# Performance work log

Measured on AMD Instinct MI355X. Metric: run time of the kernel, lower is better.

## Reference

```python
import jax, jax.numpy as jnp
import numpy as np

HIDDEN = 1024
NUM_HEADS = 8
HEAD_DIM = HIDDEN // NUM_HEADS
ROPE_BASE = 10000.0
RMS_EPS = 1e-6


def _rotate_half(x):
    # interleaved rotate: (x0,x1,x2,x3,...) -> (-x1,x0,-x3,x2,...)
    x1 = x[..., ::2]
    x2 = x[..., 1::2]
    return jnp.stack([-x2, x1], axis=-1).reshape(x.shape)


def _rope_cos_sin(seq_len, rotary_dim, dtype):
    inv_freq = 1.0 / (ROPE_BASE ** (jnp.arange(0, rotary_dim, 2, dtype=jnp.float32) / rotary_dim))
    pos = jnp.arange(seq_len, dtype=jnp.float32)
    freqs = pos[:, None] * inv_freq[None, :]            # [S, rd/2]
    cos = jnp.repeat(jnp.cos(freqs), 2, axis=-1)        # [S, rd]
    sin = jnp.repeat(jnp.sin(freqs), 2, axis=-1)
    return cos.astype(dtype)[None, None], sin.astype(dtype)[None, None]


def setup_inputs() -> dict:
    key = jax.random.key(0)
    k = jax.random.split(key, 8)
    B, S, H = 2, 2048, HIDDEN
    hidden_states = jax.random.normal(k[0], (B, S, H), dtype=jnp.float32)
    attention_mask = jax.random.randint(k[1], (B, S, S), 0, 2) > 0
    rel_ts_bias = jax.random.normal(k[2], (B, S, S), dtype=jnp.float32)
    s1 = 1.0 / np.sqrt(H)
    W_qkvu = jax.random.normal(k[3], (H, H * 6), dtype=jnp.float32) * s1
    W_out = jax.random.normal(k[4], (H * 3, H), dtype=jnp.float32) * (1.0 / np.sqrt(H * 3))
    b_out = jnp.zeros((H,), dtype=jnp.float32)
    rms_weight = jnp.ones((H,), dtype=jnp.float32)
    return {"hidden_states": hidden_states, "attention_mask": attention_mask,
            "rel_ts_bias": rel_ts_bias, "W_qkvu": W_qkvu, "W_out": W_out,
            "b_out": b_out, "rms_weight": rms_weight}


def reference(hidden_states, attention_mask, rel_ts_bias, W_qkvu, W_out, b_out, rms_weight):
    B, S, H = hidden_states.shape
    nh, hd = NUM_HEADS, HEAD_DIM
    fused = jax.nn.silu(hidden_states @ W_qkvu)          # [B,S,6H]
    gated = fused[..., :3 * H]                            # [B,S,3H]
    v = fused[..., 3 * H:4 * H].reshape(B, S, nh, hd).transpose(0, 2, 1, 3)
    q = fused[..., 4 * H:5 * H].reshape(B, S, nh, hd).transpose(0, 2, 1, 3)
    kk = fused[..., 5 * H:].reshape(B, S, nh, hd).transpose(0, 2, 1, 3)

    cos, sin = _rope_cos_sin(S, hd, hidden_states.dtype)  # rotary_dim == head_dim
    q_rope = q * cos + _rotate_half(q) * sin
    k_rope = kk * cos + _rotate_half(kk) * sin

    inv_s = 1.0 / max(S, 1)
    qk = jax.nn.relu(jnp.einsum('bhnd,bhmd->bhnm', q, kk)) * inv_s
    qk_rope = jax.nn.relu(jnp.einsum('bhnd,bhmd->bhnm', q_rope, k_rope)) * inv_s

    mask = attention_mask[:, None]                        # [B,1,S,S]
    qk = jnp.where(mask, qk, 0.0)
    qk_rope = jnp.where(mask, qk_rope, 0.0)
    ts_bias = jnp.where(attention_mask, rel_ts_bias, 0.0)

    ts_out = jnp.einsum('bnm,bhmd->bnhd', ts_bias, v)
    rope_out = jnp.einsum('bhnm,bhmd->bnhd', qk_rope, v)
    plain_out = jnp.einsum('bhnm,bhmd->bnhd', qk, v)

    combined = jnp.concatenate([rope_out, ts_out, plain_out], axis=-1).reshape(B, S, 3 * H)
    out = (combined * gated) @ W_out + b_out
    y = out + hidden_states
    rms = jax.lax.rsqrt(jnp.mean(y * y, axis=-1, keepdims=True) + RMS_EPS)
    return y * rms * rms_weight
```

## Files before the change

### kernel.cpp

```cpp
#include <hip/hip_runtime.h>
#include <math.h>

static constexpr int Bz = 2;
static constexpr int Sq = 2048;
static constexpr int Hh = 1024;
static constexpr int NH = 8;
static constexpr int HD = 128;
static constexpr int H3 = 3072;
static constexpr int H6 = 6144;

typedef unsigned short ushort_t;
typedef float f32x4v __attribute__((ext_vector_type(4)));
typedef short s16x8 __attribute__((ext_vector_type(8)));

static constexpr size_t FUSED_OFF = 0;
static constexpr size_t A2_OFF    = 12582912;
static constexpr size_t HB_OFF    = 18874368;
static constexpr size_t MTB_OFF   = 18874368;
static constexpr size_t WQT_OFF   = 20971520;
static constexpr size_t WOT_OFF   = 24117248;
static constexpr size_t QR_OFF    = 25690112;
static constexpr size_t KR_OFF    = 27787264;
static constexpr size_t VT_OFF    = 29884416;
static constexpr size_t TAB_OFF   = 31981568;
static constexpr size_t FLAG_OFF  = 32243712;
static constexpr size_t TSB_OFF   = 32243716;

__device__ __forceinline__ float silu_(float x) { return x / (1.0f + expf(-x)); }
__device__ __forceinline__ ushort_t f2bf(float x) {
  unsigned int u = __float_as_uint(x);
  u += 0x7fffu + ((u >> 16) & 1u);
  return (ushort_t)(u >> 16);
}
__device__ __forceinline__ float bf2f(ushort_t u) {
  return __uint_as_float(((unsigned int)u) << 16);
}
__device__ __forceinline__ void g2l16(const ushort_t* g, ushort_t* l) {
  __builtin_amdgcn_global_load_lds(
      (const __attribute__((address_space(1))) unsigned int*)g,
      (__attribute__((address_space(3))) unsigned int*)l, 16, 0, 0);
}

__global__ __launch_bounds__(256) void hstu_mask_detect(const unsigned int* __restrict__ m,
                                                        int* __restrict__ flag) {
  __shared__ int s_any;
  if (threadIdx.x == 0) s_any = 0;
  __syncthreads();
  int any = 0;
  for (int i = threadIdx.x; i < 65536; i += 256)
    if (m[i] > 1u) any = 1;
  if (any) s_any = 1;
  __syncthreads();
  if (threadIdx.x == 0) *flag = s_any;
}

__global__ __launch_bounds__(256) void hstu_tab(float* __restrict__ tab) {
  int t = blockIdx.x * 256 + threadIdx.x;
  int i = t & 63;
  int s = t >> 6;
  float inv = powf(10000.0f, -(float)i / 64.0f);
  float sn, cs;
  sincosf((float)s * inv, &sn, &cs);
  tab[2 * t + 0] = cs;
  tab[2 * t + 1] = sn;
}

__global__ __launch_bounds__(256) void hstu_msk(const int* __restrict__ mask32,
                                                const unsigned char* __restrict__ mask8,
                                                const int* __restrict__ mflag,
                                                const float* __restrict__ bias,
                                                ushort_t* __restrict__ tsb,
                                                ushort_t* __restrict__ mtb) {
  const size_t base = ((size_t)blockIdx.x * 256 + threadIdx.x) * 8;
  const int m_u8 = *mflag;
  int mk[8];
  if (m_u8) {
    uchar4 a = *(const uchar4*)&mask8[base];
    uchar4 b = *(const uchar4*)&mask8[base + 4];
    mk[0] = a.x; mk[1] = a.y; mk[2] = a.z; mk[3] = a.w;
    mk[4] = b.x; mk[5] = b.y; mk[6] = b.z; mk[7] = b.w;
  } else {
    int4 a = *(const int4*)&mask32[base];
    int4 b = *(const int4*)&mask32[base + 4];
    mk[0] = a.x; mk[1] = a.y; mk[2] = a.z; mk[3] = a.w;
    mk[4] = b.x; mk[5] = b.y; mk[6] = b.z; mk[7] = b.w;
  }
  float4 b0 = *(const float4*)&bias[base];
  float4 b1 = *(const float4*)&bias[base + 4];
  float bb[8] = {b0.x, b0.y, b0.z, b0.w, b1.x, b1.y, b1.z, b1.w};
  ushort_t ts[8], mt[8];
#pragma unroll
  for (int i = 0; i < 8; ++i) {
    ts[i] = f2bf(mk[i] ? bb[i] : 0.0f);
    mt[i] = mk[i] ? 0x3f80u : 0u;
  }
  *(s16x8*)&tsb[base] = *(s16x8*)ts;
  *(s16x8*)&mtb[base] = *(s16x8*)mt;
}

__global__ __launch_bounds__(256) void hstu_cvt(const float* __restrict__ in,
                                                ushort_t* __restrict__ out, int n4) {
  int i = blockIdx.x * 256 + threadIdx.x;
  if (i >= n4) return;
  float4 v = *(const float4*)&in[(size_t)i * 4];
  ushort4 o;
  o.x = f2bf(v.x); o.y = f2bf(v.y); o.z = f2bf(v.z); o.w = f2bf(v.w);
  *(ushort4*)&out[(size_t)i * 4] = o;
}

__global__ __launch_bounds__(256) void hstu_cvt_t(const float* __restrict__ in,
                                                  ushort_t* __restrict__ out, int K, int N) {
  __shared__ float t[32][33];
  const int n0 = blockIdx.x * 32, k0 = blockIdx.y * 32;
  const int c = threadIdx.x & 31, rr = threadIdx.x >> 5;
#pragma unroll
  for (int p = 0; p < 4; ++p)
    t[rr + p * 8][c] = in[(size_t)(k0 + rr + p * 8) * N + n0 + c];
  __syncthreads();
#pragma unroll
  for (int p = 0; p < 4; ++p)
    out[(size_t)(n0 + rr + p * 8) * K + k0 + c] = f2bf(t[c][rr + p * 8]);
}

__global__ __launch_bounds__(256) void hstu_rope(const ushort_t* __restrict__ fused,
                                                 const float2* __restrict__ tab,
                                                 ushort_t* __restrict__ qr,
                                                 ushort_t* __restrict__ kr) {
  const int idx = blockIdx.x * 256 + threadIdx.x;
  const int row = idx >> 7;
  const int cg = (idx & 127) * 8;
  const int s = row & (Sq - 1);
  const float2* trow = &tab[(size_t)s * 64 + ((cg & 127) >> 1)];
  float2 t[4];
#pragma unroll
  for (int p = 0; p < 4; ++p) t[p] = trow[p];

  s16x8 q8 = *(const s16x8*)&fused[(size_t)row * H6 + 4 * Hh + cg];
  s16x8 k8 = *(const s16x8*)&fused[(size_t)row * H6 + 5 * Hh + cg];
  ushort_t qo[8], ko[8];
#pragma unroll
  for (int p = 0; p < 4; ++p) {
    float qx = bf2f((ushort_t)q8[2 * p]), qy = bf2f((ushort_t)q8[2 * p + 1]);
    float kx = bf2f((ushort_t)k8[2 * p]), ky = bf2f((ushort_t)k8[2 * p + 1]);
    qo[2 * p] = f2bf(qx * t[p].x - qy * t[p].y);
    qo[2 * p + 1] = f2bf(qy * t[p].x + qx * t[p].y);
    ko[2 * p] = f2bf(kx * t[p].x - ky * t[p].y);
    ko[2 * p + 1] = f2bf(ky * t[p].x + kx * t[p].y);
  }
  *(s16x8*)&qr[(size_t)row * Hh + cg] = *(s16x8*)qo;
  *(s16x8*)&kr[(size_t)row * Hh + cg] = *(s16x8*)ko;
}

__global__ __launch_bounds__(256) void hstu_vt(const ushort_t* __restrict__ fused,
                                               ushort_t* __restrict__ vt) {
  __shared__ ushort_t t[32][36];
  const int m0 = blockIdx.x * 32, d0 = blockIdx.y * 32, bh = blockIdx.z;
  const int b = bh >> 3, h = bh & 7;
  const int r = threadIdx.x >> 3, cg = (threadIdx.x & 7) * 4;
  *(ushort4*)&t[r][cg] =
      *(const ushort4*)&fused[(size_t)(b * Sq + m0 + r) * H6 + 3 * Hh + h * HD + d0 + cg];
  __syncthreads();
  ushort4 o;
  o.x = t[cg + 0][r]; o.y = t[cg + 1][r]; o.z = t[cg + 2][r]; o.w = t[cg + 3][r];
  *(ushort4*)&vt[(size_t)(bh * HD + d0 + r) * Sq + m0 + cg] = o;
}

__global__ __launch_bounds__(256) void hstu_gemm_silu(const ushort_t* __restrict__ A,
                                                      const ushort_t* __restrict__ Bt,
                                                      ushort_t* __restrict__ C) {
  constexpr int K = 1024, N = H6;
  __shared__ ushort_t As[128 * 64];
  __shared__ ushort_t Bs[128 * 64];
  const int tid = threadIdx.x, lane = tid & 63, wid = tid >> 6;
  const int lo4 = lane & 15, hi2 = lane >> 4;
  const int wr = wid >> 1, wc = wid & 1;
  const int row0 = blockIdx.y * 128, col0 = blockIdx.x * 128;
  const int srow = lane >> 3, scol = (lane & 7) * 8;
  f32x4v acc[4][4];
#pragma unroll
  for (int i = 0; i < 4; ++i)
#pragma unroll
    for (int j = 0; j < 4; ++j) acc[i][j] = {0.f, 0.f, 0.f, 0.f};

  for (int k0 = 0; k0 < K; k0 += 64) {
    __syncthreads();
#pragma unroll
    for (int i = 0; i < 4; ++i) {
      const int rb = wid * 32 + i * 8;
      g2l16(&A[(size_t)(row0 + rb + srow) * K + k0 + scol], &As[rb * 64]);
      g2l16(&Bt[(size_t)(col0 + rb + srow) * K + k0 + scol], &Bs[rb * 64]);
    }
    __syncthreads();
#pragma unroll
    for (int kc = 0; kc < 2; ++kc) {
      s16x8 af[4], bfr[4];
#pragma unroll
      for (int mi = 0; mi < 4; ++mi)
        af[mi] = *(const s16x8*)&As[(wr * 64 + mi * 16 + lo4) * 64 + kc * 32 + hi2 * 8];
#pragma unroll
      for (int nj = 0; nj < 4; ++nj)
        bfr[nj] = *(const s16x8*)&Bs[(wc * 64 + nj * 16 + lo4) * 64 + kc * 32 + hi2 * 8];
#pragma unroll
      for (int mi = 0; mi < 4; ++mi)
#pragma unroll
        for (int nj = 0; nj < 4; ++nj)
          acc[mi][nj] = __builtin_amdgcn_mfma_f32_16x16x32_bf16(af[mi], bfr[nj], acc[mi][nj], 0, 0, 0);
    }
  }
#pragma unroll
  for (int mi = 0; mi < 4; ++mi)
#pragma unroll
    for (int nj = 0; nj < 4; ++nj)
#pragma unroll
      for (int r = 0; r < 4; ++r) {
        const int row = row0 + wr * 64 + mi * 16 + hi2 * 4 + r;
        const int col = col0 + wc * 64 + nj * 16 + lo4;
        C[(size_t)row * N + col] = f2bf(silu_(acc[mi][nj][r]));
      }
}

__global__ __launch_bounds__(256) void hstu_gemm_out(const ushort_t* __restrict__ A,
                                                     const ushort_t* __restrict__ Bt,
                                                     const float* __restrict__ bout,
                                                     const float* __restrict__ hidden,
                                                     float* __restrict__ C) {
  constexpr int K = H3, N = Hh;
  __shared__ ushort_t As[128 * 64];
  __shared__ ushort_t Bs[64 * 64];
  const int tid = threadIdx.x, lane = tid & 63, wid = tid >> 6;
  const int lo4 = lane & 15, hi2 = lane >> 4;
  const int wr = wid >> 1, wc = wid & 1;
  const int row0 = blockIdx.y * 128, col0 = blockIdx.x * 64;
  const int srow = lane >> 3, scol = (lane & 7) * 8;
  f32x4v acc[4][2];
#pragma unroll
  for (int i = 0; i < 4; ++i)
#pragma unroll
    for (int j = 0; j < 2; ++j) acc[i][j] = {0.f, 0.f, 0.f, 0.f};

  for (int k0 = 0; k0 < K; k0 += 64) {
    __syncthreads();
#pragma unroll
    for (int i = 0; i < 4; ++i) {
      const int rb = wid * 32 + i * 8;
      g2l16(&A[(size_t)(row0 + rb + srow) * K + k0 + scol], &As[rb * 64]);
    }
#pragma unroll
    for (int i = 0; i < 2; ++i) {
      const int rb = wid * 16 + i * 8;
      g2l16(&Bt[(size_t)(col0 + rb + srow) * K + k0 + scol], &Bs[rb * 64]);
    }
    __syncthreads();
#pragma unroll
    for (int kc = 0; kc < 2; ++kc) {
      s16x8 af[4], bfr[2];
#pragma unroll
      for (int mi = 0; mi < 4; ++mi)
        af[mi] = *(const s16x8*)&As[(wr * 64 + mi * 16 + lo4) * 64 + kc * 32 + hi2 * 8];
#pragma unroll
      for (int nj = 0; nj < 2; ++nj)
        bfr[nj] = *(const s16x8*)&Bs[(wc * 32 + nj * 16 + lo4) * 64 + kc * 32 + hi2 * 8];
#pragma unroll
      for (int mi = 0; mi < 4; ++mi)
#pragma unroll
        for (int nj = 0; nj < 2; ++nj)
          acc[mi][nj] = __builtin_amdgcn_mfma_f32_16x16x32_bf16(af[mi], bfr[nj], acc[mi][nj], 0, 0, 0);
    }
  }
#pragma unroll
  for (int mi = 0; mi < 4; ++mi)
#pragma unroll
    for (int nj = 0; nj < 2; ++nj)
#pragma unroll
      for (int r = 0; r < 4; ++r) {
        const int row = row0 + wr * 64 + mi * 16 + hi2 * 4 + r;
        const int col = col0 + wc * 32 + nj * 16 + lo4;
        C[(size_t)row * N + col] = acc[mi][nj][r] + bout[col] + hidden[(size_t)row * N + col];
      }
}

__global__ __launch_bounds__(512, 4) void hstu_attn(const ushort_t* __restrict__ fused,
                                                    const ushort_t* __restrict__ qr,
                                                    const ushort_t* __restrict__ kr,
                                                    const ushort_t* __restrict__ vt,
                                                    const ushort_t* __restrict__ tsb,
                                                    const ushort_t* __restrict__ mtb,
                                                    ushort_t* __restrict__ a2) {
  __shared__ __align__(16) ushort_t Ks[32][136];
  __shared__ __align__(16) ushort_t KRs[32][136];
  __shared__ __align__(16) ushort_t Vt[128][40];
  __shared__ __align__(16) ushort_t Pl[3][64][40];
  __shared__ __align__(16) ushort_t Mt[64][40];

  const int tid = threadIdx.x;
  const int lane = tid & 63;
  const int wid = tid >> 6;
  const int lo4 = lane & 15;
  const int hi2 = lane >> 4;
  const int h = blockIdx.x;
  const int n0 = blockIdx.y * 64;
  const int b = blockIdx.z;
  const float inv_s = 1.0f / 2048.0f;

  const int krow = tid >> 4, kcol = (tid & 15) * 8;
  const int vdd = tid >> 2, vmg = (tid & 3) * 8;
  const int trow = (tid & 255) >> 2, tmg = (tid & 3) * 8;
  const ushort_t* TM = (wid < 4) ? tsb : mtb;
  const size_t kbase = (size_t)b * Sq * H6 + 5 * Hh + h * HD + kcol;
  const size_t krbase = (size_t)b * Sq * Hh + h * HD + kcol;
  const size_t vbase = (size_t)((b * NH + h) * HD + vdd) * Sq + vmg;
  const size_t tbase = (size_t)(b * Sq + n0 + trow) * Sq + tmg;

  const int t_w = wid >> 2;
  const int rq = wid & 3;
  s16x8 qf[4];
  {
    const int row = tid >> 4;
    const int colg = (tid & 15) * 8;
#pragma unroll
    for (int half = 0; half < 2; ++half) {
      const size_t gr = (size_t)(b * Sq + n0 + half * 32 + row);
      *(s16x8*)&Ks[row][colg] = *(const s16x8*)&fused[gr * H6 + 4 * Hh + h * HD + colg];
      *(s16x8*)&KRs[row][colg] = *(const s16x8*)&qr[gr * Hh + h * HD + colg];
      __syncthreads();
      if ((rq >> 1) == half) {
        const int lrow = (rq & 1) * 16 + lo4;
        const ushort_t(*Qsrc)[136] = t_w ? KRs : Ks;
#pragma unroll
        for (int c = 0; c < 4; ++c)
          qf[c] = *(const s16x8*)&Qsrc[lrow][c * 32 + hi2 * 8];
      }
      __syncthreads();
    }
  }

  const f32x4v zero4 = {0.f, 0.f, 0.f, 0.f};
  f32x4v accO[3][2][2];
#pragma unroll
  for (int t = 0; t < 3; ++t)
#pragma unroll
    for (int rt = 0; rt < 2; ++rt)
#pragma unroll
      for (int ct = 0; ct < 2; ++ct) accO[t][rt][ct] = zero4;

  const int rh2 = wid >> 2;
  const int cq = wid & 3;

  s16x8 kreg, krreg, vreg, tmreg;
#define LOADT(T)                                                            \
  {                                                                         \
    const size_t moff = (size_t)(T) * 32;                                   \
    kreg = *(const s16x8*)&fused[kbase + (moff + krow) * H6];               \
    krreg = *(const s16x8*)&kr[krbase + (moff + krow) * Hh];                \
    vreg = *(const s16x8*)&vt[vbase + moff];                                \
    tmreg = *(const s16x8*)&TM[tbase + moff];                               \
  }
#define WRITET()                                                            \
  {                                                                         \
    *(s16x8*)&Ks[krow][kcol] = kreg;                                        \
    *(s16x8*)&KRs[krow][kcol] = krreg;                                      \
    *(s16x8*)&Vt[vdd][vmg] = vreg;                                          \
    if (wid < 4) *(s16x8*)&Pl[2][trow][tmg] = tmreg;                        \
    else *(s16x8*)&Mt[trow][tmg] = tmreg;                                   \
  }

  LOADT(0);
  WRITET();
  __syncthreads();

  for (int t = 0; t < Sq / 32; ++t) {
    if (t + 1 < Sq / 32) LOADT(t + 1);
    {
      const ushort_t(*Kmat)[136] = t_w ? KRs : Ks;
#pragma unroll
      for (int mt2 = 0; mt2 < 2; ++mt2) {
        f32x4v a = zero4;
#pragma unroll
        for (int c = 0; c < 4; ++c) {
          s16x8 kf = *(const s16x8*)&Kmat[mt2 * 16 + lo4][c * 32 + hi2 * 8];
          a = __builtin_amdgcn_mfma_f32_16x16x32_bf16(qf[c], kf, a, 0, 0, 0);
        }
#pragma unroll
        for (int r = 0; r < 4; ++r) {
          const int n = rq * 16 + hi2 * 4 + r;
          const int m = mt2 * 16 + lo4;
          Pl[t_w][n][m] = f2bf(fmaxf(a[r], 0.f) * inv_s * bf2f(Mt[n][m]));
        }
      }
    }
    __syncthreads();
    {
      s16x8 af[3][2];
#pragma unroll
      for (int ty = 0; ty < 3; ++ty)
#pragma unroll
        for (int rt = 0; rt < 2; ++rt)
          af[ty][rt] = *(const s16x8*)&Pl[ty][rh2 * 32 + rt * 16 + lo4][hi2 * 8];
      s16x8 bfv[2];
#pragma unroll
      for (int ct = 0; ct < 2; ++ct)
        bfv[ct] = *(const s16x8*)&Vt[cq * 32 + ct * 16 + lo4][hi2 * 8];
#pragma unroll
      for (int ty = 0; ty < 3; ++ty)
#pragma unroll
        for (int rt = 0; rt < 2; ++rt)
#pragma unroll
          for (int ct = 0; ct < 2; ++ct)
            accO[ty][rt][ct] =
                __builtin_amdgcn_mfma_f32_16x16x32_bf16(af[ty][rt], bfv[ct], accO[ty][rt][ct], 0, 0, 0);
    }
    __syncthreads();
    if (t + 1 < Sq / 32) WRITET();
    __syncthreads();
  }
#undef LOADT
#undef WRITET

  const int toff[3] = {256, 0, 128};
#pragma unroll
  for (int ty = 0; ty < 3; ++ty)
#pragma unroll
    for (int rt = 0; rt < 2; ++rt)
#pragma unroll
      for (int ct = 0; ct < 2; ++ct)
#pragma unroll
        for (int r = 0; r < 4; ++r) {
          const int n = n0 + rh2 * 32 + rt * 16 + hi2 * 4 + r;
          const int dd = cq * 32 + ct * 16 + lo4;
          const int col3 = h * 384 + toff[ty] + dd;
          const float g = bf2f(fused[(size_t)(b * Sq + n) * H6 + col3]);
          a2[(size_t)(b * Sq + n) * H3 + col3] = f2bf(accO[ty][rt][ct][r] * g);
        }
}

__global__ __launch_bounds__(256) void hstu_rms(float* __restrict__ y,
                                                const float* __restrict__ w) {
  __shared__ float red[4];
  const int row = blockIdx.x;
  const int tid = threadIdx.x;
  float4 v = *(float4*)&y[(size_t)row * Hh + tid * 4];
  float ss = v.x * v.x + v.y * v.y + v.z * v.z + v.w * v.w;
#pragma unroll
  for (int o = 32; o > 0; o >>= 1) ss += __shfl_down(ss, o);
  if ((tid & 63) == 0) red[tid >> 6] = ss;
  __syncthreads();
  const float tot = red[0] + red[1] + red[2] + red[3];
  const float r = 1.0f / sqrtf(tot / (float)Hh + 1e-6f);
  float4 wv = *(const float4*)&w[tid * 4];
  v.x *= r * wv.x;
  v.y *= r * wv.y;
  v.z *= r * wv.z;
  v.w *= r * wv.w;
  *(float4*)&y[(size_t)row * Hh + tid * 4] = v;
}

extern "C" void kernel_launch(void* const* d_in, const int* in_sizes, int n_in,
                              void* d_out, int out_size, void* d_ws, size_t ws_size,
                              hipStream_t stream) {
  const float* hidden = (const float*)d_in[0];
  const void* mask = d_in[1];
  const float* bias = (const float*)d_in[2];
  const float* Wqkvu = (const float*)d_in[3];
  const float* Wout = (const float*)d_in[4];
  const float* bout = (const float*)d_in[5];
  const float* rmsw = (const float*)d_in[6];
  float* out = (float*)d_out;
  float* ws = (float*)d_ws;

  ushort_t* fused = (ushort_t*)(ws + FUSED_OFF);
  ushort_t* a2 = (ushort_t*)(ws + A2_OFF);
  ushort_t* hb = (ushort_t*)(ws + HB_OFF);
  ushort_t* mtbp = (ushort_t*)(ws + MTB_OFF);
  ushort_t* wqt = (ushort_t*)(ws + WQT_OFF);
  ushort_t* wot = (ushort_t*)(ws + WOT_OFF);
  ushort_t* qrb = (ushort_t*)(ws + QR_OFF);
  ushort_t* krb = (ushort_t*)(ws + KR_OFF);
  ushort_t* vtb = (ushort_t*)(ws + VT_OFF);
  float* tab = ws + TAB_OFF;
  int* mflag = (int*)(ws + FLAG_OFF);
  ushort_t* tsbp = (ushort_t*)(ws + TSB_OFF);

  hstu_mask_detect<<<1, 256, 0, stream>>>((const unsigned int*)mask, mflag);
  hstu_tab<<<512, 256, 0, stream>>>(tab);
  hstu_cvt<<<4096, 256, 0, stream>>>(hidden, hb, (Bz * Sq * Hh) / 4);
  hstu_cvt_t<<<dim3(H6 / 32, Hh / 32), 256, 0, stream>>>(Wqkvu, wqt, Hh, H6);
  hstu_cvt_t<<<dim3(Hh / 32, H3 / 32), 256, 0, stream>>>(Wout, wot, H3, Hh);
  hstu_gemm_silu<<<dim3(H6 / 128, (Bz * Sq) / 128), 256, 0, stream>>>(hb, wqt, fused);
  hstu_msk<<<(Bz * Sq * Sq / 8) / 256, 256, 0, stream>>>(
      (const int*)mask, (const unsigned char*)mask, mflag, bias, tsbp, mtbp);
  hstu_rope<<<(Bz * Sq * Hh / 8) / 256, 256, 0, stream>>>(fused, (const float2*)tab, qrb, krb);
  hstu_vt<<<dim3(Sq / 32, HD / 32, Bz * NH), 256, 0, stream>>>(fused, vtb);
  hstu_attn<<<dim3(NH, Sq / 64, Bz), 512, 0, stream>>>(fused, qrb, krb, vtb, tsbp, mtbp, a2);
  hstu_gemm_out<<<dim3(Hh / 64, (Bz * Sq) / 128), 256, 0, stream>>>(a2, wot, bout, hidden, out);
  hstu_rms<<<Bz * Sq, 256, 0, stream>>>(out, rmsw);
}
```

Before: 367.2 us.

## Split attention tile loads into two staged groups and drop one barrier per tile

Splits the per-tile global loads into two groups. K, rotated K and mask are prefetched early and written to shared memory after the PV MFMAs. V and the ts-bias tile are fetched after the mid-iteration barrier and written at the start of the next iteration. This removes one __syncthreads per tile iteration, lets global loads overlap with both MFMA phases, and adds s_setprio around the MFMA loops. The 1/S scale is folded into the bf16 mask value, which removes one multiply per score; this is exact because 1/2048 is a power of two.

```diff
diff --git a/kernel.cpp b/kernel.cpp
--- a/kernel.cpp
+++ b/kernel.cpp
@@ -73,6 +73,7 @@
                                                 ushort_t* __restrict__ mtb) {
   const size_t base = ((size_t)blockIdx.x * 256 + threadIdx.x) * 8;
   const int m_u8 = *mflag;
+  const ushort_t ivs = f2bf(1.0f / 2048.0f);
   int mk[8];
   if (m_u8) {
     uchar4 a = *(const uchar4*)&mask8[base];
@@ -92,7 +93,7 @@
 #pragma unroll
   for (int i = 0; i < 8; ++i) {
     ts[i] = f2bf(mk[i] ? bb[i] : 0.0f);
-    mt[i] = mk[i] ? 0x3f80u : 0u;
+    mt[i] = mk[i] ? ivs : 0u;
   }
   *(s16x8*)&tsb[base] = *(s16x8*)ts;
   *(s16x8*)&mtb[base] = *(s16x8*)mt;
@@ -300,12 +301,13 @@
   const int h = blockIdx.x;
   const int n0 = blockIdx.y * 64;
   const int b = blockIdx.z;
-  const float inv_s = 1.0f / 2048.0f;
+  constexpr int NT = Sq / 32;
 
   const int krow = tid >> 4, kcol = (tid & 15) * 8;
   const int vdd = tid >> 2, vmg = (tid & 3) * 8;
   const int trow = (tid & 255) >> 2, tmg = (tid & 3) * 8;
-  const ushort_t* TM = (wid < 4) ? tsb : mtb;
+  const bool ts_role = (wid < 4);
+  const ushort_t* TM = ts_role ? tsb : mtb;
   const size_t kbase = (size_t)b * Sq * H6 + 5 * Hh + h * HD + kcol;
   const size_t krbase = (size_t)b * Sq * Hh + h * HD + kcol;
   const size_t vbase = (size_t)((b * NH + h) * HD + vdd) * Sq + vmg;
@@ -347,48 +349,61 @@
   const int cq = wid & 3;
 
   s16x8 kreg, krreg, vreg, tmreg;
-#define LOADT(T)                                                            \
+#define LOAD_G2(T)                                                          \
   {                                                                         \
     const size_t moff = (size_t)(T) * 32;                                   \
     kreg = *(const s16x8*)&fused[kbase + (moff + krow) * H6];               \
     krreg = *(const s16x8*)&kr[krbase + (moff + krow) * Hh];                \
-    vreg = *(const s16x8*)&vt[vbase + moff];                                \
-    tmreg = *(const s16x8*)&TM[tbase + moff];                               \
-  }
-#define WRITET()                                                            \
+    if (!ts_role) tmreg = *(const s16x8*)&TM[tbase + moff];                 \
+  }
+#define WRITE_G2()                                                          \
   {                                                                         \
     *(s16x8*)&Ks[krow][kcol] = kreg;                                        \
     *(s16x8*)&KRs[krow][kcol] = krreg;                                      \
+    if (!ts_role) *(s16x8*)&Mt[trow][tmg] = tmreg;                          \
+  }
+#define LOAD_G1(T)                                                          \
+  {                                                                         \
+    const size_t moff = (size_t)(T) * 32;                                   \
+    vreg = *(const s16x8*)&vt[vbase + moff];                                \
+    if (ts_role) tmreg = *(const s16x8*)&TM[tbase + moff];                  \
+  }
+#define WRITE_G1()                                                          \
+  {                                                                         \
     *(s16x8*)&Vt[vdd][vmg] = vreg;                                          \
-    if (wid < 4) *(s16x8*)&Pl[2][trow][tmg] = tmreg;                        \
-    else *(s16x8*)&Mt[trow][tmg] = tmreg;                                   \
-  }
-
-  LOADT(0);
-  WRITET();
+    if (ts_role) *(s16x8*)&Pl[2][trow][tmg] = tmreg;                        \
+  }
+
+  LOAD_G2(0);
+  WRITE_G2();
+  LOAD_G1(0);
   __syncthreads();
 
-  for (int t = 0; t < Sq / 32; ++t) {
-    if (t + 1 < Sq / 32) LOADT(t + 1);
+  for (int t = 0; t < NT; ++t) {
+    if (t + 1 < NT) LOAD_G2(t + 1);
+    WRITE_G1();
     {
       const ushort_t(*Kmat)[136] = t_w ? KRs : Ks;
 #pragma unroll
       for (int mt2 = 0; mt2 < 2; ++mt2) {
         f32x4v a = zero4;
+        __builtin_amdgcn_s_setprio(1);
 #pragma unroll
         for (int c = 0; c < 4; ++c) {
           s16x8 kf = *(const s16x8*)&Kmat[mt2 * 16 + lo4][c * 32 + hi2 * 8];
           a = __builtin_amdgcn_mfma_f32_16x16x32_bf16(qf[c], kf, a, 0, 0, 0);
         }
+        __builtin_amdgcn_s_setprio(0);
 #pragma unroll
         for (int r = 0; r < 4; ++r) {
           const int n = rq * 16 + hi2 * 4 + r;
           const int m = mt2 * 16 + lo4;
-          Pl[t_w][n][m] = f2bf(fmaxf(a[r], 0.f) * inv_s * bf2f(Mt[n][m]));
+          Pl[t_w][n][m] = f2bf(fmaxf(a[r], 0.f) * bf2f(Mt[n][m]));
         }
       }
     }
     __syncthreads();
+    if (t + 1 < NT) LOAD_G1(t + 1);
     {
       s16x8 af[3][2];
 #pragma unroll
@@ -400,6 +415,7 @@
 #pragma unroll
       for (int ct = 0; ct < 2; ++ct)
         bfv[ct] = *(const s16x8*)&Vt[cq * 32 + ct * 16 + lo4][hi2 * 8];
+      __builtin_amdgcn_s_setprio(1);
 #pragma unroll
       for (int ty = 0; ty < 3; ++ty)
 #pragma unroll
@@ -408,13 +424,15 @@
           for (int ct = 0; ct < 2; ++ct)
             accO[ty][rt][ct] =
                 __builtin_amdgcn_mfma_f32_16x16x32_bf16(af[ty][rt], bfv[ct], accO[ty][rt][ct], 0, 0, 0);
-    }
+      __builtin_amdgcn_s_setprio(0);
+    }
+    if (t + 1 < NT) WRITE_G2();
     __syncthreads();
-    if (t + 1 < Sq / 32) WRITET();
-    __syncthreads();
-  }
-#undef LOADT
-#undef WRITET
+  }
+#undef LOAD_G2
+#undef WRITE_G2
+#undef LOAD_G1
+#undef WRITE_G1
 
   const int toff[3] = {256, 0, 128};
 #pragma unroll
```

Result: slower. 376.8 us (+2.6%).

## Restructure attention kernel with 32x32 MFMA, 64-wide key tiles, byte mask

Applied to the files above, without the earlier changes.

Rewrites the attention kernel to process 64-key tiles per iteration using 32x32x16 bf16 MFMA instead of 16x16x32, cutting loop iterations and barriers. The timestamp-bias operand is now loaded directly from global memory into registers as an MFMA A fragment rather than staged through LDS. The mask is stored as one byte per element instead of a bf16 0/1 value, halving mask traffic. The register-prefetch pipeline of the old loop is replaced by direct global-to-LDS staging after a barrier, which may expose more load latency, and the larger LDS tiles may reduce occupancy.

```diff
diff --git a/kernel.cpp b/kernel.cpp
--- a/kernel.cpp
+++ b/kernel.cpp
@@ -11,6 +11,7 @@
 
 typedef unsigned short ushort_t;
 typedef float f32x4v __attribute__((ext_vector_type(4)));
+typedef float f32x16v __attribute__((ext_vector_type(16)));
 typedef short s16x8 __attribute__((ext_vector_type(8)));
 
 static constexpr size_t FUSED_OFF = 0;
@@ -70,7 +71,7 @@
                                                 const int* __restrict__ mflag,
                                                 const float* __restrict__ bias,
                                                 ushort_t* __restrict__ tsb,
-                                                ushort_t* __restrict__ mtb) {
+                                                unsigned char* __restrict__ mtb8) {
   const size_t base = ((size_t)blockIdx.x * 256 + threadIdx.x) * 8;
   const int m_u8 = *mflag;
   int mk[8];
@@ -88,14 +89,15 @@
   float4 b0 = *(const float4*)&bias[base];
   float4 b1 = *(const float4*)&bias[base + 4];
   float bb[8] = {b0.x, b0.y, b0.z, b0.w, b1.x, b1.y, b1.z, b1.w};
-  ushort_t ts[8], mt[8];
+  ushort_t ts[8];
+  unsigned char mo[8];
 #pragma unroll
   for (int i = 0; i < 8; ++i) {
     ts[i] = f2bf(mk[i] ? bb[i] : 0.0f);
-    mt[i] = mk[i] ? 0x3f80u : 0u;
+    mo[i] = mk[i] ? 1u : 0u;
   }
   *(s16x8*)&tsb[base] = *(s16x8*)ts;
-  *(s16x8*)&mtb[base] = *(s16x8*)mt;
+  *(uint2*)&mtb8[base] = *(uint2*)mo;
 }
 
 __global__ __launch_bounds__(256) void hstu_cvt(const float* __restrict__ in,
@@ -284,153 +286,146 @@
                                                     const ushort_t* __restrict__ kr,
                                                     const ushort_t* __restrict__ vt,
                                                     const ushort_t* __restrict__ tsb,
-                                                    const ushort_t* __restrict__ mtb,
+                                                    const unsigned char* __restrict__ mtb8,
                                                     ushort_t* __restrict__ a2) {
-  __shared__ __align__(16) ushort_t Ks[32][136];
-  __shared__ __align__(16) ushort_t KRs[32][136];
-  __shared__ __align__(16) ushort_t Vt[128][40];
-  __shared__ __align__(16) ushort_t Pl[3][64][40];
-  __shared__ __align__(16) ushort_t Mt[64][40];
+  __shared__ __align__(16) ushort_t Ks[64][136];
+  __shared__ __align__(16) ushort_t KRs[64][136];
+  __shared__ __align__(16) ushort_t Vt[128][72];
+  __shared__ __align__(16) ushort_t Pl[2][64][72];
+  __shared__ __align__(16) unsigned char Mt[64][72];
 
   const int tid = threadIdx.x;
   const int lane = tid & 63;
   const int wid = tid >> 6;
-  const int lo4 = lane & 15;
-  const int hi2 = lane >> 4;
+  const int l31 = lane & 31;
+  const int khalf = lane >> 5;
   const int h = blockIdx.x;
   const int n0 = blockIdx.y * 64;
   const int b = blockIdx.z;
-  const float inv_s = 1.0f / 2048.0f;
-
-  const int krow = tid >> 4, kcol = (tid & 15) * 8;
-  const int vdd = tid >> 2, vmg = (tid & 3) * 8;
-  const int trow = (tid & 255) >> 2, tmg = (tid & 3) * 8;
-  const ushort_t* TM = (wid < 4) ? tsb : mtb;
-  const size_t kbase = (size_t)b * Sq * H6 + 5 * Hh + h * HD + kcol;
-  const size_t krbase = (size_t)b * Sq * Hh + h * HD + kcol;
-  const size_t vbase = (size_t)((b * NH + h) * HD + vdd) * Sq + vmg;
-  const size_t tbase = (size_t)(b * Sq + n0 + trow) * Sq + tmg;
+  const float ivs = 1.0f / 2048.0f;
+  constexpr int NT = Sq / 64;
 
   const int t_w = wid >> 2;
-  const int rq = wid & 3;
-  s16x8 qf[4];
+  const int nq = (wid >> 1) & 1;
+  const int mq = wid & 1;
+  const int nh = wid & 1;
+  const int dq = wid >> 1;
+
+#define STAGE_QQR()                                                              \
+  {                                                                              \
+    _Pragma("unroll") for (int p = 0; p < 2; ++p) {                              \
+      const int row = (tid >> 4) + p * 32;                                       \
+      const int col = (tid & 15) * 8;                                            \
+      const size_t gr = (size_t)(b * Sq + n0 + row);                             \
+      *(s16x8*)&Ks[row][col] = *(const s16x8*)&fused[gr * H6 + 4 * Hh + h * HD + col]; \
+      *(s16x8*)&KRs[row][col] = *(const s16x8*)&qr[gr * Hh + h * HD + col];      \
+    }                                                                            \
+  }
+#define STAGE_KKR(T)                                                             \
+  {                                                                              \
+    _Pragma("unroll") for (int p = 0; p < 2; ++p) {                              \
+      const int row = (tid >> 4) + p * 32;                                       \
+      const int col = (tid & 15) * 8;                                            \
+      const size_t gr = (size_t)(b * Sq + (T) * 64 + row);                       \
+      *(s16x8*)&Ks[row][col] = *(const s16x8*)&fused[gr * H6 + 5 * Hh + h * HD + col]; \
+      *(s16x8*)&KRs[row][col] = *(const s16x8*)&kr[gr * Hh + h * HD + col];      \
+    }                                                                            \
+  }
+#define STAGE_MT(T)                                                              \
+  {                                                                              \
+    const int row = tid >> 3;                                                    \
+    const int c8 = (tid & 7) * 8;                                                \
+    *(uint2*)&Mt[row][c8] =                                                      \
+        *(const uint2*)&mtb8[(size_t)(b * Sq + n0 + row) * Sq + (T) * 64 + c8];  \
+  }
+#define STAGE_VT(T)                                                              \
+  {                                                                              \
+    _Pragma("unroll") for (int p = 0; p < 2; ++p) {                              \
+      const int dd = (tid >> 3) + p * 64;                                        \
+      const int mcol = (tid & 7) * 8;                                            \
+      *(s16x8*)&Vt[dd][mcol] =                                                   \
+          *(const s16x8*)&vt[(size_t)((b * NH + h) * HD + dd) * Sq + (T) * 64 + mcol]; \
+    }                                                                            \
+  }
+
+  STAGE_QQR();
+  __syncthreads();
+  s16x8 qf[8];
   {
-    const int row = tid >> 4;
-    const int colg = (tid & 15) * 8;
-#pragma unroll
-    for (int half = 0; half < 2; ++half) {
-      const size_t gr = (size_t)(b * Sq + n0 + half * 32 + row);
-      *(s16x8*)&Ks[row][colg] = *(const s16x8*)&fused[gr * H6 + 4 * Hh + h * HD + colg];
-      *(s16x8*)&KRs[row][colg] = *(const s16x8*)&qr[gr * Hh + h * HD + colg];
-      __syncthreads();
-      if ((rq >> 1) == half) {
-        const int lrow = (rq & 1) * 16 + lo4;
-        const ushort_t(*Qsrc)[136] = t_w ? KRs : Ks;
-#pragma unroll
-        for (int c = 0; c < 4; ++c)
-          qf[c] = *(const s16x8*)&Qsrc[lrow][c * 32 + hi2 * 8];
-      }
-      __syncthreads();
-    }
-  }
-
-  const f32x4v zero4 = {0.f, 0.f, 0.f, 0.f};
-  f32x4v accO[3][2][2];
-#pragma unroll
-  for (int t = 0; t < 3; ++t)
-#pragma unroll
-    for (int rt = 0; rt < 2; ++rt)
-#pragma unroll
-      for (int ct = 0; ct < 2; ++ct) accO[t][rt][ct] = zero4;
-
-  const int rh2 = wid >> 2;
-  const int cq = wid & 3;
-
-  s16x8 kreg, krreg, vreg, tmreg;
-#define LOADT(T)                                                            \
-  {                                                                         \
-    const size_t moff = (size_t)(T) * 32;                                   \
-    kreg = *(const s16x8*)&fused[kbase + (moff + krow) * H6];               \
-    krreg = *(const s16x8*)&kr[krbase + (moff + krow) * Hh];                \
-    vreg = *(const s16x8*)&vt[vbase + moff];                                \
-    tmreg = *(const s16x8*)&TM[tbase + moff];                               \
-  }
-#define WRITET()                                                            \
-  {                                                                         \
-    *(s16x8*)&Ks[krow][kcol] = kreg;                                        \
-    *(s16x8*)&KRs[krow][kcol] = krreg;                                      \
-    *(s16x8*)&Vt[vdd][vmg] = vreg;                                          \
-    if (wid < 4) *(s16x8*)&Pl[2][trow][tmg] = tmreg;                        \
-    else *(s16x8*)&Mt[trow][tmg] = tmreg;                                   \
-  }
-
-  LOADT(0);
-  WRITET();
-  __syncthreads();
-
-  for (int t = 0; t < Sq / 32; ++t) {
-    if (t + 1 < Sq / 32) LOADT(t + 1);
+    const ushort_t(*Qsrc)[136] = t_w ? KRs : Ks;
+#pragma unroll
+    for (int ks = 0; ks < 8; ++ks)
+      qf[ks] = *(const s16x8*)&Qsrc[nq * 32 + l31][ks * 16 + khalf * 8];
+  }
+  __syncthreads();
+  STAGE_KKR(0);
+  STAGE_MT(0);
+  __syncthreads();
+
+  f32x16v acc0 = {0.f, 0.f, 0.f, 0.f, 0.f, 0.f, 0.f, 0.f,
+                  0.f, 0.f, 0.f, 0.f, 0.f, 0.f, 0.f, 0.f};
+  f32x16v acc1 = acc0;
+  f32x16v acc2 = acc0;
+
+  const size_t tsrow = (size_t)(b * Sq + n0 + nh * 32 + l31) * Sq;
+
+  for (int t = 0; t < NT; ++t) {
+    const int m0 = t * 64;
+    STAGE_VT(t);
+    s16x8 tsf[4];
+#pragma unroll
+    for (int ks = 0; ks < 4; ++ks)
+      tsf[ks] = *(const s16x8*)&tsb[tsrow + m0 + ks * 16 + khalf * 8];
     {
       const ushort_t(*Kmat)[136] = t_w ? KRs : Ks;
-#pragma unroll
-      for (int mt2 = 0; mt2 < 2; ++mt2) {
-        f32x4v a = zero4;
-#pragma unroll
-        for (int c = 0; c < 4; ++c) {
-          s16x8 kf = *(const s16x8*)&Kmat[mt2 * 16 + lo4][c * 32 + hi2 * 8];
-          a = __builtin_amdgcn_mfma_f32_16x16x32_bf16(qf[c], kf, a, 0, 0, 0);
-        }
-#pragma unroll
-        for (int r = 0; r < 4; ++r) {
-          const int n = rq * 16 + hi2 * 4 + r;
-          const int m = mt2 * 16 + lo4;
-          Pl[t_w][n][m] = f2bf(fmaxf(a[r], 0.f) * inv_s * bf2f(Mt[n][m]));
-        }
+      f32x16v sacc = {0.f, 0.f, 0.f, 0.f, 0.f, 0.f, 0.f, 0.f,
+                      0.f, 0.f, 0.f, 0.f, 0.f, 0.f, 0.f, 0.f};
+#pragma unroll
+      for (int ks = 0; ks < 8; ++ks) {
+        s16x8 bfr = *(const s16x8*)&Kmat[mq * 32 + l31][ks * 16 + khalf * 8];
+        sacc = __builtin_amdgcn_mfma_f32_32x32x16_bf16(qf[ks], bfr, sacc, 0, 0, 0);
       }
-    }
-    __syncthreads();
-    {
-      s16x8 af[3][2];
-#pragma unroll
-      for (int ty = 0; ty < 3; ++ty)
-#pragma unroll
-        for (int rt = 0; rt < 2; ++rt)
-          af[ty][rt] = *(const s16x8*)&Pl[ty][rh2 * 32 + rt * 16 + lo4][hi2 * 8];
-      s16x8 bfv[2];
-#pragma unroll
-      for (int ct = 0; ct < 2; ++ct)
-        bfv[ct] = *(const s16x8*)&Vt[cq * 32 + ct * 16 + lo4][hi2 * 8];
-#pragma unroll
-      for (int ty = 0; ty < 3; ++ty)
-#pragma unroll
-        for (int rt = 0; rt < 2; ++rt)
-#pragma unroll
-          for (int ct = 0; ct < 2; ++ct)
-            accO[ty][rt][ct] =
-                __builtin_amdgcn_mfma_f32_16x16x32_bf16(af[ty][rt], bfv[ct], accO[ty][rt][ct], 0, 0, 0);
-    }
-    __syncthreads();
-    if (t + 1 < Sq / 32) WRITET();
-    __syncthreads();
-  }
-#undef LOADT
-#undef WRITET
-
-  const int toff[3] = {256, 0, 128};
-#pragma unroll
-  for (int ty = 0; ty < 3; ++ty)
-#pragma unroll
-    for (int rt = 0; rt < 2; ++rt)
-#pragma unroll
-      for (int ct = 0; ct < 2; ++ct)
-#pragma unroll
-        for (int r = 0; r < 4; ++r) {
-          const int n = n0 + rh2 * 32 + rt * 16 + hi2 * 4 + r;
-          const int dd = cq * 32 + ct * 16 + lo4;
-          const int col3 = h * 384 + toff[ty] + dd;
-          const float g = bf2f(fused[(size_t)(b * Sq + n) * H6 + col3]);
-          a2[(size_t)(b * Sq + n) * H3 + col3] = f2bf(accO[ty][rt][ct][r] * g);
-        }
+      const int m = mq * 32 + l31;
+#pragma unroll
+      for (int r = 0; r < 16; ++r) {
+        const int n = nq * 32 + (r & 3) + 8 * (r >> 2) + 4 * khalf;
+        const float val = Mt[n][m] ? fmaxf(sacc[r], 0.f) * ivs : 0.f;
+        Pl[t_w][n][m] = f2bf(val);
+      }
+    }
+    __syncthreads();
+    if (t + 1 < NT) {
+      STAGE_KKR(t + 1);
+      STAGE_MT(t + 1);
+    }
+#pragma unroll
+    for (int ks = 0; ks < 4; ++ks) {
+      s16x8 bV = *(const s16x8*)&Vt[dq * 32 + l31][ks * 16 + khalf * 8];
+      s16x8 aP0 = *(const s16x8*)&Pl[0][nh * 32 + l31][ks * 16 + khalf * 8];
+      s16x8 aP1 = *(const s16x8*)&Pl[1][nh * 32 + l31][ks * 16 + khalf * 8];
+      acc0 = __builtin_amdgcn_mfma_f32_32x32x16_bf16(aP0, bV, acc0, 0, 0, 0);
+      acc1 = __builtin_amdgcn_mfma_f32_32x32x16_bf16(aP1, bV, acc1, 0, 0, 0);
+      acc2 = __builtin_amdgcn_mfma_f32_32x32x16_bf16(tsf[ks], bV, acc2, 0, 0, 0);
+    }
+    __syncthreads();
+  }
+#undef STAGE_QQR
+#undef STAGE_KKR
+#undef STAGE_MT
+#undef STAGE_VT
+
+  const int dd = dq * 32 + l31;
+#pragma unroll
+  for (int r = 0; r < 16; ++r) {
+    const int n = n0 + nh * 32 + (r & 3) + 8 * (r >> 2) + 4 * khalf;
+    const size_t rowb = (size_t)(b * Sq + n);
+    const int c_pl = h * 384 + 256 + dd;
+    const int c_ro = h * 384 + 0 + dd;
+    const int c_ts = h * 384 + 128 + dd;
+    a2[rowb * H3 + c_pl] = f2bf(acc0[r] * bf2f(fused[rowb * H6 + c_pl]));
+    a2[rowb * H3 + c_ro] = f2bf(acc1[r] * bf2f(fused[rowb * H6 + c_ro]));
+    a2[rowb * H3 + c_ts] = f2bf(acc2[r] * bf2f(fused[rowb * H6 + c_ts]));
+  }
 }
 
 __global__ __launch_bounds__(256) void hstu_rms(float* __restrict__ y,
@@ -470,7 +465,7 @@
   ushort_t* fused = (ushort_t*)(ws + FUSED_OFF);
   ushort_t* a2 = (ushort_t*)(ws + A2_OFF);
   ushort_t* hb = (ushort_t*)(ws + HB_OFF);
-  ushort_t* mtbp = (ushort_t*)(ws + MTB_OFF);
+  unsigned char* mtb8 = (unsigned char*)(ws + MTB_OFF);
   ushort_t* wqt = (ushort_t*)(ws + WQT_OFF);
   ushort_t* wot = (ushort_t*)(ws + WOT_OFF);
   ushort_t* qrb = (ushort_t*)(ws + QR_OFF);
@@ -487,10 +482,10 @@
   hstu_cvt_t<<<dim3(Hh / 32, H3 / 32), 256, 0, stream>>>(Wout, wot, H3, Hh);
   hstu_gemm_silu<<<dim3(H6 / 128, (Bz * Sq) / 128), 256, 0, stream>>>(hb, wqt, fused);
   hstu_msk<<<(Bz * Sq * Sq / 8) / 256, 256, 0, stream>>>(
-      (const int*)mask, (const unsigned char*)mask, mflag, bias, tsbp, mtbp);
+      (const int*)mask, (const unsigned char*)mask, mflag, bias, tsbp, mtb8);
   hstu_rope<<<(Bz * Sq * Hh / 8) / 256, 256, 0, stream>>>(fused, (const float2*)tab, qrb, krb);
   hstu_vt<<<dim3(Sq / 32, HD / 32, Bz * NH), 256, 0, stream>>>(fused, vtb);
-  hstu_attn<<<dim3(NH, Sq / 64, Bz), 512, 0, stream>>>(fused, qrb, krb, vtb, tsbp, mtbp, a2);
+  hstu_attn<<<dim3(NH, Sq / 64, Bz), 512, 0, stream>>>(fused, qrb, krb, vtb, tsbp, mtb8, a2);
   hstu_gemm_out<<<dim3(Hh / 64, (Bz * Sq) / 128), 256, 0, stream>>>(a2, wot, bout, hidden, out);
   hstu_rms<<<Bz * Sq, 256, 0, stream>>>(out, rmsw);
 }
```

Result: no change. 371.3 us (+1.1%).
